# Optimization experiments

Measured on AMD Instinct MI355X. Metric: run time of the kernel, lower is better.

The kernel has to match this reference:

```python
import jax, jax.numpy as jnp
import numpy as np

N = 200000      # active voxels
K = 27          # kernel volume (3x3x3)
M = 50000       # rulebook pairs per kernel offset
CIN = 64
COUT = 64


def setup_inputs() -> dict:
    key = jax.random.key(0)
    k1, k2, k3, k4 = jax.random.split(key, 4)
    feats = jax.random.normal(k1, (N, CIN), dtype=jnp.float32)
    std = 1.0 / np.sqrt(CIN * K)
    kernel = jax.random.uniform(k2, (K, CIN, COUT), dtype=jnp.float32,
                                minval=-std, maxval=std)
    in_map = jax.random.randint(k3, (K, M), 0, N, dtype=jnp.int32)
    out_map = jax.random.randint(k4, (K, M), 0, N, dtype=jnp.int32)
    return {"feats": feats, "kernel": kernel, "in_map": in_map, "out_map": out_map}


def reference(feats, kernel, in_map, out_map):
    # gather: [K, M, Cin]
    gathered = feats[in_map]
    # per-offset GEMM: [K, M, Cout]
    partial = jnp.einsum('kmi,kio->kmo', gathered, kernel)
    # scatter-add into output features [N, Cout]
    out = jnp.zeros((feats.shape[0], kernel.shape[-1]), dtype=feats.dtype)
    out = out.at[out_map].add(partial)
    return out
```

## Files before the change

### kernel.cpp

```cpp
#include <hip/hip_runtime.h>
#include <hip/hip_fp16.h>

#define CIN   64
#define COUT  64

typedef __attribute__((ext_vector_type(8))) short bf16x8;
typedef __attribute__((ext_vector_type(4))) float f32x4;

__device__ inline unsigned short f2bf(float f) {
    unsigned u = __float_as_uint(f);
    return (unsigned short)((u + 0x7FFFu + ((u >> 16) & 1u)) >> 16);
}

__device__ inline unsigned pack_h2(float lo, float hi) {
    __half l = __float2half(lo), h = __float2half(hi);
    return (unsigned)__half_as_ushort(l) | ((unsigned)__half_as_ushort(h) << 16);
}

__global__ __launch_bounds__(256)
void cvt_hist(const float4* __restrict__ in, unsigned short* __restrict__ outb,
              int n8, const int* __restrict__ out_map, int total,
              int* __restrict__ cnt) {
    int i = blockIdx.x * 256 + threadIdx.x;
    if (i < n8) {
        float4 f0 = in[2 * i], f1 = in[2 * i + 1];
        bf16x8 o;
        o[0] = (short)f2bf(f0.x); o[1] = (short)f2bf(f0.y);
        o[2] = (short)f2bf(f0.z); o[3] = (short)f2bf(f0.w);
        o[4] = (short)f2bf(f1.x); o[5] = (short)f2bf(f1.y);
        o[6] = (short)f2bf(f1.z); o[7] = (short)f2bf(f1.w);
        *(bf16x8*)(outb + 8 * (size_t)i) = o;
    }
    if (i < total)
        atomicAdd(&cnt[out_map[i]], 1);
}

__global__ __launch_bounds__(256)
void scanA(const int* __restrict__ cnt, int* __restrict__ excl,
           int* __restrict__ blocksum, int N) {
    __shared__ int sm[256];
    const int b = blockIdx.x, t = threadIdx.x;
    const int base = b * 1024 + t * 4;
    int v0 = (base + 0 < N) ? cnt[base + 0] : 0;
    int v1 = (base + 1 < N) ? cnt[base + 1] : 0;
    int v2 = (base + 2 < N) ? cnt[base + 2] : 0;
    int v3 = (base + 3 < N) ? cnt[base + 3] : 0;
    const int s = v0 + v1 + v2 + v3;
    sm[t] = s; __syncthreads();
    for (int off = 1; off < 256; off <<= 1) {
        int x = (t >= off) ? sm[t - off] : 0;
        __syncthreads();
        sm[t] += x;
        __syncthreads();
    }
    const int e = sm[t] - s;
    if (t == 255) blocksum[b] = sm[t];
    if (base + 0 < N) excl[base + 0] = e;
    if (base + 1 < N) excl[base + 1] = e + v0;
    if (base + 2 < N) excl[base + 2] = e + v0 + v1;
    if (base + 3 < N) excl[base + 3] = e + v0 + v1 + v2;
}

__global__ __launch_bounds__(256)
void scanB(const int* __restrict__ blocksum, int* __restrict__ blockbase,
           int nb, int* __restrict__ total_out) {
    __shared__ int sm[256];
    const int t = threadIdx.x;
    const int s = (t < nb) ? blocksum[t] : 0;
    sm[t] = s; __syncthreads();
    for (int off = 1; off < 256; off <<= 1) {
        int x = (t >= off) ? sm[t - off] : 0;
        __syncthreads();
        sm[t] += x;
        __syncthreads();
    }
    if (t < nb) blockbase[t] = sm[t] - s;
    if (t == 255) *total_out = sm[255];
}

__global__ __launch_bounds__(256)
void scanC(int* __restrict__ offsets, int* __restrict__ ofs_work,
           const int* __restrict__ blockbase, int N) {
    int i = blockIdx.x * 256 + threadIdx.x;
    if (i >= N) return;
    const int v = offsets[i] + blockbase[i >> 10];
    offsets[i]  = v;
    ofs_work[i] = v;
}

__global__ __launch_bounds__(256)
void spconv_phase1(const unsigned short* __restrict__ featsb,
                   const float*          __restrict__ weight,
                   const int*            __restrict__ in_map,
                   const int*            __restrict__ out_map,
                   int*                  __restrict__ ofs_work,
                   unsigned*             __restrict__ partial_dw,
                   int M) {
    const int k      = blockIdx.y;
    const int tid    = threadIdx.x;
    const int lane   = tid & 63;
    const int m      = lane & 15;
    const int quad   = lane >> 4;
    const int wave   = blockIdx.x * 4 + (tid >> 6);
    const int nwaves = gridDim.x * 4;
    const bool odd   = (m & 1);

    const float* __restrict__ wk = weight + (size_t)k * (CIN * COUT);
    bf16x8 bfrag[4][2];
#pragma unroll
    for (int t = 0; t < 4; ++t)
#pragma unroll
        for (int h = 0; h < 2; ++h) {
            const int n  = 16 * t + m;
            const int c0 = 32 * h + 8 * quad;
#pragma unroll
            for (int j = 0; j < 8; ++j)
                bfrag[t][h][j] = (short)f2bf(wk[(c0 + j) * COUT + n]);
        }

    const int base   = k * M;
    const int ntiles = M >> 4;

    int    tile = wave;
    int    cur_slt = 0;
    bf16x8 cur_a0 = {}, cur_a1 = {};
    if (tile < ntiles) {
        const int p0 = tile << 4;
        const int in_row  = in_map[base + p0 + m];
        const int out_row = out_map[base + p0 + m];
        if (quad == 0) cur_slt = atomicAdd(&ofs_work[out_row], 1);
        const unsigned short* fb = featsb + ((size_t)in_row << 6) + 8 * quad;
        cur_a0 = *(const bf16x8*)fb;
        cur_a1 = *(const bf16x8*)(fb + 32);
    }

    while (tile < ntiles) {
        const int next = tile + nwaves;
        int    nxt_slt = 0;
        bf16x8 nxt_a0 = {}, nxt_a1 = {};
        if (next < ntiles) {
            const int np0 = next << 4;
            const int n_in  = in_map[base + np0 + m];
            const int n_out = out_map[base + np0 + m];
            if (quad == 0) nxt_slt = atomicAdd(&ofs_work[n_out], 1);
            const unsigned short* fb = featsb + ((size_t)n_in << 6) + 8 * quad;
            nxt_a0 = *(const bf16x8*)fb;
            nxt_a1 = *(const bf16x8*)(fb + 32);
        }

        f32x4 acc[4];
#pragma unroll
        for (int t = 0; t < 4; ++t) {
            acc[t] = {0.f, 0.f, 0.f, 0.f};
            acc[t] = __builtin_amdgcn_mfma_f32_16x16x32_bf16(cur_a0, bfrag[t][0], acc[t], 0, 0, 0);
            acc[t] = __builtin_amdgcn_mfma_f32_16x16x32_bf16(cur_a1, bfrag[t][1], acc[t], 0, 0, 0);
        }

        const int row0  = 4 * quad + (odd ? 2 : 0);
        const int s0    = __shfl(cur_slt, row0);
        const int s1    = __shfl(cur_slt, row0 + 1);
        const int coldw = m >> 1;
#pragma unroll
        for (int t = 0; t < 4; ++t) {
            const float send0 = odd ? acc[t][0] : acc[t][2];
            const float send1 = odd ? acc[t][1] : acc[t][3];
            const float recv0 = __shfl_xor(send0, 1);
            const float recv1 = __shfl_xor(send1, 1);

            const unsigned d0 = odd ? pack_h2(recv0, acc[t][2])
                                    : pack_h2(acc[t][0], recv0);
            const unsigned d1 = odd ? pack_h2(recv1, acc[t][3])
                                    : pack_h2(acc[t][1], recv1);

            partial_dw[(size_t)s0 * 32 + coldw + 8 * t] = d0;
            partial_dw[(size_t)s1 * 32 + coldw + 8 * t] = d1;
        }

        tile    = next;
        cur_slt = nxt_slt;
        cur_a0  = nxt_a0;
        cur_a1  = nxt_a1;
    }
}

__global__ __launch_bounds__(256)
void spconv_phase2(const unsigned* __restrict__ partial_dw,
                   const int*      __restrict__ offsets,
                   float2*         __restrict__ out,
                   int nrows) {
    const int tid  = threadIdx.x;
    const int lane = tid & 63;
    const int half = lane >> 5;
    const int c2   = lane & 31;
    const int wave = blockIdx.x * 4 + (tid >> 6);
    const int nw   = gridDim.x * 4;

    if (wave >= nrows) return;
    int cur_s = offsets[wave];
    int cur_e = offsets[wave + 1];

    for (int r = wave; r < nrows; r += nw) {
        const int start = cur_s;
        const int c     = cur_e - start;
        const int rn    = r + nw;
        if (rn < nrows) {
            cur_s = offsets[rn];
            cur_e = offsets[rn + 1];
        }

        float ax = 0.f, ay = 0.f;
        for (int j0 = 0; j0 < c; j0 += 8) {
#pragma unroll
            for (int u = 0; u < 4; ++u) {
                const int j = j0 + 2 * u + half;
                if (j < c) {
                    const unsigned v = partial_dw[(size_t)(start + j) * 32 + c2];
                    ax += __half2float(__ushort_as_half((unsigned short)(v & 0xFFFF)));
                    ay += __half2float(__ushort_as_half((unsigned short)(v >> 16)));
                }
            }
        }

        ax += __shfl_xor(ax, 32);
        ay += __shfl_xor(ay, 32);
        if (half == 0)
            out[(size_t)r * 32 + c2] = make_float2(ax, ay);
    }
}

__global__ __launch_bounds__(256)
void spconv_atomic(const float* __restrict__ feats,
                   const float* __restrict__ weight,
                   const int*   __restrict__ in_map,
                   const int*   __restrict__ out_map,
                   float*       __restrict__ out,
                   int M) {
    const int k      = blockIdx.y;
    const int tid    = threadIdx.x;
    const int lane   = tid & 63;
    const int m      = lane & 15;
    const int quad   = lane >> 4;
    const int wave   = blockIdx.x * 4 + (tid >> 6);
    const int nwaves = gridDim.x * 4;

    const float* __restrict__ wk = weight + (size_t)k * (CIN * COUT);
    bf16x8 bfrag[4][2];
#pragma unroll
    for (int t = 0; t < 4; ++t)
#pragma unroll
        for (int h = 0; h < 2; ++h) {
            const int n  = 16 * t + m;
            const int c0 = 32 * h + 8 * quad;
#pragma unroll
            for (int j = 0; j < 8; ++j)
                bfrag[t][h][j] = (short)f2bf(wk[(c0 + j) * COUT + n]);
        }

    const int base   = k * M;
    const int ntiles = M >> 4;

    for (int tile = wave; tile < ntiles; tile += nwaves) {
        const int p0 = tile << 4;
        const int in_row  = in_map[base + p0 + m];
        const int out_row = out_map[base + p0 + m];

        const float* __restrict__ fr = feats + ((size_t)in_row << 6) + 8 * quad;
        const f32x4 f0 = *(const f32x4*)(fr + 0);
        const f32x4 f1 = *(const f32x4*)(fr + 4);
        const f32x4 f2 = *(const f32x4*)(fr + 32);
        const f32x4 f3 = *(const f32x4*)(fr + 36);

        bf16x8 a0, a1;
#pragma unroll
        for (int j = 0; j < 4; ++j) {
            a0[j]     = (short)f2bf(f0[j]);
            a0[j + 4] = (short)f2bf(f1[j]);
            a1[j]     = (short)f2bf(f2[j]);
            a1[j + 4] = (short)f2bf(f3[j]);
        }

        int orow[4];
#pragma unroll
        for (int r = 0; r < 4; ++r)
            orow[r] = __shfl(out_row, 4 * quad + r);

        f32x4 acc[4];
#pragma unroll
        for (int t = 0; t < 4; ++t) {
            acc[t] = {0.f, 0.f, 0.f, 0.f};
            acc[t] = __builtin_amdgcn_mfma_f32_16x16x32_bf16(a0, bfrag[t][0], acc[t], 0, 0, 0);
            acc[t] = __builtin_amdgcn_mfma_f32_16x16x32_bf16(a1, bfrag[t][1], acc[t], 0, 0, 0);
        }

#pragma unroll
        for (int t = 0; t < 4; ++t)
#pragma unroll
            for (int r = 0; r < 4; ++r)
                atomicAdd(out + (size_t)orow[r] * COUT + 16 * t + m, acc[t][r]);
    }
}

__global__ __launch_bounds__(256)
void zero_out_kernel(float4* __restrict__ out, int n4) {
    int i = blockIdx.x * 256 + threadIdx.x;
    if (i < n4) out[i] = make_float4(0.f, 0.f, 0.f, 0.f);
}

static inline size_t al256(size_t x) { return (x + 255) & ~(size_t)255; }

extern "C" void kernel_launch(void* const* d_in, const int* in_sizes, int n_in,
                              void* d_out, int out_size, void* d_ws, size_t ws_size,
                              hipStream_t stream) {
    const float* feats   = (const float*)d_in[0];
    const float* weight  = (const float*)d_in[1];
    const int*   in_map  = (const int*)d_in[2];
    const int*   out_map = (const int*)d_in[3];
    float*       out     = (float*)d_out;

    const int K     = in_sizes[1] / (CIN * COUT);
    const int M     = in_sizes[2] / K;
    const int N     = out_size / COUT;
    const int total = K * M;
    const int nb    = (N + 1023) >> 10;

    const size_t off_b  = al256((size_t)(N + 1) * 4);
    const size_t work_b = al256((size_t)N * 4);
    const size_t bs_b   = al256((size_t)nb * 4);
    const size_t bb_b   = al256((size_t)nb * 4);
    const size_t fb_b   = al256((size_t)N * CIN * 2);
    const size_t part_b = (size_t)total * COUT * 2;
    const size_t need   = off_b + work_b + bs_b + bb_b + fb_b + part_b;

    if ((M & 15) == 0 && nb <= 256 && ws_size >= need) {
        char* p = (char*)d_ws;
        int*            offsets   = (int*)p;            p += off_b;
        int*            ofs_work  = (int*)p;            p += work_b;
        int*            blocksum  = (int*)p;            p += bs_b;
        int*            blockbase = (int*)p;            p += bb_b;
        unsigned short* featsb    = (unsigned short*)p; p += fb_b;
        unsigned*       partial   = (unsigned*)p;

        const int n8 = N * CIN / 8;
        const int fused_n = (n8 > total) ? n8 : total;

        hipMemsetAsync(ofs_work, 0, (size_t)N * 4, stream);
        cvt_hist<<<(fused_n + 255) / 256, 256, 0, stream>>>(
            (const float4*)feats, featsb, n8, out_map, total, ofs_work);
        scanA<<<nb, 256, 0, stream>>>(ofs_work, offsets, blocksum, N);
        scanB<<<1, 256, 0, stream>>>(blocksum, blockbase, nb, offsets + N);
        scanC<<<(N + 255) / 256, 256, 0, stream>>>(offsets, ofs_work, blockbase, N);

        dim3 g1(80, K);
        spconv_phase1<<<g1, 256, 0, stream>>>(featsb, weight, in_map, out_map,
                                              ofs_work, partial, M);

        spconv_phase2<<<8192, 256, 0, stream>>>(partial, offsets, (float2*)out, N);
        return;
    }

    int n4 = out_size / 4;
    zero_out_kernel<<<(n4 + 255) / 256, 256, 0, stream>>>((float4*)out, n4);
    dim3 grid(80, K);
    spconv_atomic<<<grid, 256, 0, stream>>>(feats, weight, in_map, out_map, out, M);
}
```

Before: 328.1 us.

## Record per-pair ranks in histogram pass, deepen phase1 prefetch, vectorize phase2 reads

The histogram kernel now stores each pair's atomic return value as a rank, so phase1 computes its slot as offsets[out_row] + rank instead of doing a second atomicAdd on a work copy of the offsets. Phase1 now prefetches map indices two tiles ahead and feature rows one tile ahead, which is meant to hide gather latency. Phase2 reads 16-byte chunks per lane with 8 rows in flight and reduces across lane groups with shuffles. The cost is an extra rank array of total*4 bytes written and read back.

```diff
diff --git a/kernel.cpp b/kernel.cpp
--- a/kernel.cpp
+++ b/kernel.cpp
@@ -17,10 +17,16 @@
     return (unsigned)__half_as_ushort(l) | ((unsigned)__half_as_ushort(h) << 16);
 }
 
+__device__ inline float2 h2f2(unsigned v) {
+    return make_float2(
+        __half2float(__ushort_as_half((unsigned short)(v & 0xFFFFu))),
+        __half2float(__ushort_as_half((unsigned short)(v >> 16))));
+}
+
 __global__ __launch_bounds__(256)
 void cvt_hist(const float4* __restrict__ in, unsigned short* __restrict__ outb,
               int n8, const int* __restrict__ out_map, int total,
-              int* __restrict__ cnt) {
+              int* __restrict__ cnt, int* __restrict__ rk) {
     int i = blockIdx.x * 256 + threadIdx.x;
     if (i < n8) {
         float4 f0 = in[2 * i], f1 = in[2 * i + 1];
@@ -32,7 +38,7 @@
         *(bf16x8*)(outb + 8 * (size_t)i) = o;
     }
     if (i < total)
-        atomicAdd(&cnt[out_map[i]], 1);
+        rk[i] = atomicAdd(&cnt[out_map[i]], 1);
 }
 
 __global__ __launch_bounds__(256)
@@ -79,13 +85,10 @@
 }
 
 __global__ __launch_bounds__(256)
-void scanC(int* __restrict__ offsets, int* __restrict__ ofs_work,
-           const int* __restrict__ blockbase, int N) {
+void scanC(int* __restrict__ offsets, const int* __restrict__ blockbase, int N) {
     int i = blockIdx.x * 256 + threadIdx.x;
     if (i >= N) return;
-    const int v = offsets[i] + blockbase[i >> 10];
-    offsets[i]  = v;
-    ofs_work[i] = v;
+    offsets[i] += blockbase[i >> 10];
 }
 
 __global__ __launch_bounds__(256)
@@ -93,7 +96,8 @@
                    const float*          __restrict__ weight,
                    const int*            __restrict__ in_map,
                    const int*            __restrict__ out_map,
-                   int*                  __restrict__ ofs_work,
+                   const int*            __restrict__ offsets,
+                   const int*            __restrict__ rk,
                    unsigned*             __restrict__ partial_dw,
                    int M) {
     const int k      = blockIdx.y;
@@ -121,44 +125,51 @@
     const int base   = k * M;
     const int ntiles = M >> 4;
 
-    int    tile = wave;
-    int    cur_slt = 0;
-    bf16x8 cur_a0 = {}, cur_a1 = {};
-    if (tile < ntiles) {
-        const int p0 = tile << 4;
-        const int in_row  = in_map[base + p0 + m];
-        const int out_row = out_map[base + p0 + m];
-        if (quad == 0) cur_slt = atomicAdd(&ofs_work[out_row], 1);
-        const unsigned short* fb = featsb + ((size_t)in_row << 6) + 8 * quad;
-        cur_a0 = *(const bf16x8*)fb;
-        cur_a1 = *(const bf16x8*)(fb + 32);
-    }
-
-    while (tile < ntiles) {
-        const int next = tile + nwaves;
-        int    nxt_slt = 0;
-        bf16x8 nxt_a0 = {}, nxt_a1 = {};
-        if (next < ntiles) {
-            const int np0 = next << 4;
-            const int n_in  = in_map[base + np0 + m];
-            const int n_out = out_map[base + np0 + m];
-            if (quad == 0) nxt_slt = atomicAdd(&ofs_work[n_out], 1);
-            const unsigned short* fb = featsb + ((size_t)n_in << 6) + 8 * quad;
-            nxt_a0 = *(const bf16x8*)fb;
-            nxt_a1 = *(const bf16x8*)(fb + 32);
+    int t0 = wave, t1 = wave + nwaves, t2 = wave + 2 * nwaves;
+
+    int ir0 = 0, orow0 = 0, rk0 = 0;
+    if (t0 < ntiles) {
+        const int p = base + (t0 << 4) + m;
+        ir0 = in_map[p]; orow0 = out_map[p]; rk0 = rk[p];
+    }
+    int slt0 = 0; bf16x8 a0_0 = {}, a1_0 = {};
+    if (t0 < ntiles) {
+        if (quad == 0) slt0 = offsets[orow0] + rk0;
+        const unsigned short* fb = featsb + ((size_t)ir0 << 6) + 8 * quad;
+        a0_0 = *(const bf16x8*)fb;
+        a1_0 = *(const bf16x8*)(fb + 32);
+    }
+    int ir1 = 0, orow1 = 0, rk1 = 0;
+    if (t1 < ntiles) {
+        const int p = base + (t1 << 4) + m;
+        ir1 = in_map[p]; orow1 = out_map[p]; rk1 = rk[p];
+    }
+
+    while (t0 < ntiles) {
+        int slt1 = 0; bf16x8 a0_1 = {}, a1_1 = {};
+        if (t1 < ntiles) {
+            if (quad == 0) slt1 = offsets[orow1] + rk1;
+            const unsigned short* fb = featsb + ((size_t)ir1 << 6) + 8 * quad;
+            a0_1 = *(const bf16x8*)fb;
+            a1_1 = *(const bf16x8*)(fb + 32);
+        }
+        int ir2 = 0, orow2 = 0, rk2 = 0;
+        if (t2 < ntiles) {
+            const int p = base + (t2 << 4) + m;
+            ir2 = in_map[p]; orow2 = out_map[p]; rk2 = rk[p];
         }
 
         f32x4 acc[4];
 #pragma unroll
         for (int t = 0; t < 4; ++t) {
             acc[t] = {0.f, 0.f, 0.f, 0.f};
-            acc[t] = __builtin_amdgcn_mfma_f32_16x16x32_bf16(cur_a0, bfrag[t][0], acc[t], 0, 0, 0);
-            acc[t] = __builtin_amdgcn_mfma_f32_16x16x32_bf16(cur_a1, bfrag[t][1], acc[t], 0, 0, 0);
+            acc[t] = __builtin_amdgcn_mfma_f32_16x16x32_bf16(a0_0, bfrag[t][0], acc[t], 0, 0, 0);
+            acc[t] = __builtin_amdgcn_mfma_f32_16x16x32_bf16(a1_0, bfrag[t][1], acc[t], 0, 0, 0);
         }
 
         const int row0  = 4 * quad + (odd ? 2 : 0);
-        const int s0    = __shfl(cur_slt, row0);
-        const int s1    = __shfl(cur_slt, row0 + 1);
+        const int s0    = __shfl(slt0, row0);
+        const int s1    = __shfl(slt0, row0 + 1);
         const int coldw = m >> 1;
 #pragma unroll
         for (int t = 0; t < 4; ++t) {
@@ -176,22 +187,21 @@
             partial_dw[(size_t)s1 * 32 + coldw + 8 * t] = d1;
         }
 
-        tile    = next;
-        cur_slt = nxt_slt;
-        cur_a0  = nxt_a0;
-        cur_a1  = nxt_a1;
-    }
-}
-
-__global__ __launch_bounds__(256)
-void spconv_phase2(const unsigned* __restrict__ partial_dw,
-                   const int*      __restrict__ offsets,
-                   float2*         __restrict__ out,
+        t0 = t1; t1 = t2; t2 += nwaves;
+        slt0 = slt1; a0_0 = a0_1; a1_0 = a1_1;
+        ir1 = ir2; orow1 = orow2; rk1 = rk2;
+    }
+}
+
+__global__ __launch_bounds__(256)
+void spconv_phase2(const uint4* __restrict__ partial_q,
+                   const int*   __restrict__ offsets,
+                   float4*      __restrict__ out4,
                    int nrows) {
     const int tid  = threadIdx.x;
     const int lane = tid & 63;
-    const int half = lane >> 5;
-    const int c2   = lane & 31;
+    const int g    = lane >> 3;
+    const int q    = lane & 7;
     const int wave = blockIdx.x * 4 + (tid >> 6);
     const int nw   = gridDim.x * 4;
 
@@ -208,23 +218,31 @@
             cur_e = offsets[rn + 1];
         }
 
-        float ax = 0.f, ay = 0.f;
+        float s0 = 0.f, s1 = 0.f, s2 = 0.f, s3 = 0.f;
+        float s4 = 0.f, s5 = 0.f, s6 = 0.f, s7 = 0.f;
         for (int j0 = 0; j0 < c; j0 += 8) {
-#pragma unroll
-            for (int u = 0; u < 4; ++u) {
-                const int j = j0 + 2 * u + half;
-                if (j < c) {
-                    const unsigned v = partial_dw[(size_t)(start + j) * 32 + c2];
-                    ax += __half2float(__ushort_as_half((unsigned short)(v & 0xFFFF)));
-                    ay += __half2float(__ushort_as_half((unsigned short)(v >> 16)));
-                }
+            const int j = j0 + g;
+            if (j < c) {
+                const uint4 v = partial_q[(size_t)(start + j) * 8 + q];
+                const float2 f0 = h2f2(v.x), f1 = h2f2(v.y);
+                const float2 f2 = h2f2(v.z), f3 = h2f2(v.w);
+                s0 += f0.x; s1 += f0.y; s2 += f1.x; s3 += f1.y;
+                s4 += f2.x; s5 += f2.y; s6 += f3.x; s7 += f3.y;
             }
         }
 
-        ax += __shfl_xor(ax, 32);
-        ay += __shfl_xor(ay, 32);
-        if (half == 0)
-            out[(size_t)r * 32 + c2] = make_float2(ax, ay);
+#pragma unroll
+        for (int msk = 8; msk <= 32; msk <<= 1) {
+            s0 += __shfl_xor(s0, msk); s1 += __shfl_xor(s1, msk);
+            s2 += __shfl_xor(s2, msk); s3 += __shfl_xor(s3, msk);
+            s4 += __shfl_xor(s4, msk); s5 += __shfl_xor(s5, msk);
+            s6 += __shfl_xor(s6, msk); s7 += __shfl_xor(s7, msk);
+        }
+
+        if (g == 0) {
+            out4[(size_t)r * 16 + 2 * q]     = make_float4(s0, s1, s2, s3);
+            out4[(size_t)r * 16 + 2 * q + 1] = make_float4(s4, s5, s6, s7);
+        }
     }
 }
 
@@ -324,37 +342,40 @@
     const int nb    = (N + 1023) >> 10;
 
     const size_t off_b  = al256((size_t)(N + 1) * 4);
-    const size_t work_b = al256((size_t)N * 4);
+    const size_t cnt_b  = al256((size_t)N * 4);
     const size_t bs_b   = al256((size_t)nb * 4);
     const size_t bb_b   = al256((size_t)nb * 4);
+    const size_t rank_b = al256((size_t)total * 4);
     const size_t fb_b   = al256((size_t)N * CIN * 2);
     const size_t part_b = (size_t)total * COUT * 2;
-    const size_t need   = off_b + work_b + bs_b + bb_b + fb_b + part_b;
+    const size_t need   = off_b + cnt_b + bs_b + bb_b + rank_b + fb_b + part_b;
 
     if ((M & 15) == 0 && nb <= 256 && ws_size >= need) {
         char* p = (char*)d_ws;
         int*            offsets   = (int*)p;            p += off_b;
-        int*            ofs_work  = (int*)p;            p += work_b;
+        int*            cnt       = (int*)p;            p += cnt_b;
         int*            blocksum  = (int*)p;            p += bs_b;
         int*            blockbase = (int*)p;            p += bb_b;
+        int*            rk        = (int*)p;            p += rank_b;
         unsigned short* featsb    = (unsigned short*)p; p += fb_b;
         unsigned*       partial   = (unsigned*)p;
 
         const int n8 = N * CIN / 8;
         const int fused_n = (n8 > total) ? n8 : total;
 
-        hipMemsetAsync(ofs_work, 0, (size_t)N * 4, stream);
+        hipMemsetAsync(cnt, 0, (size_t)N * 4, stream);
         cvt_hist<<<(fused_n + 255) / 256, 256, 0, stream>>>(
-            (const float4*)feats, featsb, n8, out_map, total, ofs_work);
-        scanA<<<nb, 256, 0, stream>>>(ofs_work, offsets, blocksum, N);
+            (const float4*)feats, featsb, n8, out_map, total, cnt, rk);
+        scanA<<<nb, 256, 0, stream>>>(cnt, offsets, blocksum, N);
         scanB<<<1, 256, 0, stream>>>(blocksum, blockbase, nb, offsets + N);
-        scanC<<<(N + 255) / 256, 256, 0, stream>>>(offsets, ofs_work, blockbase, N);
+        scanC<<<(N + 255) / 256, 256, 0, stream>>>(offsets, blockbase, N);
 
         dim3 g1(80, K);
         spconv_phase1<<<g1, 256, 0, stream>>>(featsb, weight, in_map, out_map,
-                                              ofs_work, partial, M);
-
-        spconv_phase2<<<8192, 256, 0, stream>>>(partial, offsets, (float2*)out, N);
+                                              offsets, rk, partial, M);
+
+        spconv_phase2<<<8192, 256, 0, stream>>>((const uint4*)partial, offsets,
+                                                (float4*)out, N);
         return;
     }
 
```

Measured after the change: 302.1 us. -7.9%, faster.
